# Kernel tuning notes

Measured on AMD Instinct MI355X. Metric: run time of the kernel, lower is better.

Reference implementation:

```python
import math
import jax, jax.numpy as jnp
import numpy as np

B, T, C = 2, 2048, 1024
H, HKV, HD = 16, 4, 64  # n_head, n_kv_head, head_dim
G = H // HKV            # GQA groups
WS = 1024               # sliding window size
GATE_CH = 32


def setup_inputs() -> dict:
    key = jax.random.key(0)
    ks = jax.random.split(key, 8)
    x = jax.random.normal(ks[0], (B, T, C), dtype=jnp.float32)
    ve = jax.random.normal(ks[1], (B, T, HKV * HD), dtype=jnp.float32)
    # realistic RoPE tables: half head_dim frequencies
    d = HD // 2
    inv_freq = 1.0 / (10000.0 ** (jnp.arange(d, dtype=jnp.float32) / d))
    angles = jnp.arange(T, dtype=jnp.float32)[:, None] * inv_freq[None, :]  # (T, d)
    cos = jnp.cos(angles)[None, :, None, :]  # (1, T, 1, d)
    sin = jnp.sin(angles)[None, :, None, :]
    s = 0.02
    Wq = s * jax.random.normal(ks[2], (C, H * HD), dtype=jnp.float32)
    Wk = s * jax.random.normal(ks[3], (C, HKV * HD), dtype=jnp.float32)
    Wv = s * jax.random.normal(ks[4], (C, HKV * HD), dtype=jnp.float32)
    Wproj = s * jax.random.normal(ks[5], (C, C), dtype=jnp.float32)
    Wg = s * jax.random.normal(ks[6], (GATE_CH, HKV), dtype=jnp.float32)
    return {"x": x, "ve": ve, "cos": cos, "sin": sin,
            "Wq": Wq, "Wk": Wk, "Wv": Wv, "Wproj": Wproj, "Wg": Wg, "ws": WS}


def _rope(u, cos, sin):
    d = u.shape[-1] // 2
    u1, u2 = u[..., :d], u[..., d:]
    return jnp.concatenate([u1 * cos + u2 * sin, -u1 * sin + u2 * cos], axis=-1)


def _rmsnorm(u):
    eps = jnp.finfo(u.dtype).eps
    return u * jax.lax.rsqrt(jnp.mean(u * u, axis=-1, keepdims=True) + eps)


def reference(x, ve, cos, sin, Wq, Wk, Wv, Wproj, Wg, ws):
    b, t, c = x.shape
    q = (x @ Wq).reshape(b, t, H, HD)
    k = (x @ Wk).reshape(b, t, HKV, HD)
    v = (x @ Wv).reshape(b, t, HKV, HD)
    # value-embedding gate: 2*sigmoid over first 32 channels of x
    gate = 2.0 * jax.nn.sigmoid(x[..., :GATE_CH] @ Wg)  # (b, t, HKV)
    v = v + gate[..., None] * ve.reshape(b, t, HKV, HD)
    q = _rmsnorm(_rope(q, cos, sin))
    k = _rmsnorm(_rope(k, cos, sin))
    # GQA: view q as (b, t, HKV, G, HD), contract against shared k/v per kv-head
    qg = q.reshape(b, t, HKV, G, HD)
    scale = 1.0 / math.sqrt(HD)
    scores = jnp.einsum('bqhgd,bkhd->bhgqk', qg, k) * scale  # (b, HKV, G, t, t)
    pos = jnp.arange(t)
    # key j attends iff i - ws + 1 <= j <= i (sliding causal window)
    mask = (pos[None, :] >= pos[:, None] - ws + 1) & (pos[None, :] <= pos[:, None])
    scores = jnp.where(mask[None, None, None], scores, -jnp.inf)
    attn = jax.nn.softmax(scores, axis=-1)
    y = jnp.einsum('bhgqk,bkhd->bqhgd', attn, v).reshape(b, t, H * HD)
    return y @ Wproj
```

## Files before the change

kernel.cpp:

```cpp
#include <hip/hip_runtime.h>
#include <hip/hip_bf16.h>

#define Bq 2
#define Tq 2048
#define Cq 1024
#define Hq 16
#define HKVq 4
#define HDq 64
#define Gq 4
#define WSq 1024
#define GATE_CHq 32

typedef __attribute__((ext_vector_type(8))) short short8;
typedef __attribute__((ext_vector_type(4))) float f32x4;
typedef __attribute__((ext_vector_type(2))) unsigned int u32x2;
typedef unsigned int u32;
typedef unsigned short u16;

#if __has_builtin(__builtin_amdgcn_exp2f)
#define EXP2(x) __builtin_amdgcn_exp2f(x)
#else
#define EXP2(x) exp2f(x)
#endif

__device__ __forceinline__ u16 f2bf(float f) {
  u32 u = __float_as_uint(f);
  u32 r = (u + 0x7FFFu + ((u >> 16) & 1u)) >> 16;
  return (u16)r;
}
__device__ __forceinline__ float bf2f(u16 u) {
  return __uint_as_float(((u32)u) << 16);
}

__device__ __forceinline__ void gl_lds16(const u16* g, u16* l) {
  __builtin_amdgcn_global_load_lds(
      (const u32 __attribute__((address_space(1)))*)g,
      (u32 __attribute__((address_space(3)))*)l, 16, 0, 0);
}

template <bool BF16OUT>
__global__ __launch_bounds__(256) void gemm_bt(
    const u16* __restrict__ A, const u16* __restrict__ Bt,
    void* __restrict__ Cv, int M, int N, int K) {
  __shared__ __attribute__((aligned(16))) u16 As[64 * 32];
  __shared__ __attribute__((aligned(16))) u16 Bs[128 * 32];

  const int bm0 = blockIdx.y * 64, bn0 = blockIdx.x * 128;
  const int tid = threadIdx.x;
  const int w = tid >> 6, lane = tid & 63;
  const int wm = (w >> 1) * 32, wn = (w & 1) * 64;
  const int quad = lane >> 4, l16 = lane & 15;

  f32x4 acc[2][4];
#pragma unroll
  for (int mt = 0; mt < 2; mt++)
#pragma unroll
    for (int nt = 0; nt < 4; nt++) acc[mt][nt] = (f32x4){0.f, 0.f, 0.f, 0.f};

  const int mA = tid >> 2, gpA = tid & 3;
  const int goffA = mA * K + (gpA ^ ((mA >> 1) & 3)) * 8;
  int goffB[2];
#pragma unroll
  for (int i = 0; i < 2; i++) {
    int s = i * 256 + tid;
    int m = s >> 2, gp = s & 3;
    goffB[i] = m * K + (gp ^ ((m >> 1) & 3)) * 8;
  }
  const u16* Ab = A + (long)bm0 * K;
  const u16* Bb = Bt + (long)bn0 * K;

  const u16* pA[2];
  const u16* pB[4];
#pragma unroll
  for (int t = 0; t < 2; t++) {
    int ml = wm + t * 16 + l16;
    pA[t] = &As[(ml * 4 + (quad ^ ((ml >> 1) & 3))) * 8];
  }
#pragma unroll
  for (int t = 0; t < 4; t++) {
    int nl = wn + t * 16 + l16;
    pB[t] = &Bs[(nl * 4 + (quad ^ ((nl >> 1) & 3))) * 8];
  }

  for (int k0 = 0; k0 < K; k0 += 32) {
    __syncthreads();
    gl_lds16(Ab + goffA + k0, &As[(w * 64) * 8]);
#pragma unroll
    for (int i = 0; i < 2; i++)
      gl_lds16(Bb + goffB[i] + k0, &Bs[(i * 256 + w * 64) * 8]);
    __syncthreads();

    short8 af[2], bf[4];
#pragma unroll
    for (int t = 0; t < 2; t++) af[t] = *(const short8*)pA[t];
#pragma unroll
    for (int t = 0; t < 4; t++) bf[t] = *(const short8*)pB[t];
#pragma unroll
    for (int mt = 0; mt < 2; mt++)
#pragma unroll
      for (int nt = 0; nt < 4; nt++)
        acc[mt][nt] = __builtin_amdgcn_mfma_f32_16x16x32_bf16(
            af[mt], bf[nt], acc[mt][nt], 0, 0, 0);
  }

#pragma unroll
  for (int mt = 0; mt < 2; mt++)
#pragma unroll
    for (int nt = 0; nt < 4; nt++) {
      int row0 = bm0 + wm + mt * 16 + quad * 4;
      int col = bn0 + wn + nt * 16 + l16;
#pragma unroll
      for (int r = 0; r < 4; r++) {
        if (BF16OUT)
          ((u16*)Cv)[(long)(row0 + r) * N + col] = f2bf(acc[mt][nt][r]);
        else
          ((float*)Cv)[(long)(row0 + r) * N + col] = acc[mt][nt][r];
      }
    }
}

__global__ __launch_bounds__(256) void cast_bf16(const float* __restrict__ S,
                                                 u16* __restrict__ D) {
  int i = (blockIdx.x * 256 + threadIdx.x) * 8;
  float4 a = *(const float4*)(S + i);
  float4 b = *(const float4*)(S + i + 4);
  union { short8 v; u16 u[8]; } o;
  o.u[0] = f2bf(a.x); o.u[1] = f2bf(a.y); o.u[2] = f2bf(a.z); o.u[3] = f2bf(a.w);
  o.u[4] = f2bf(b.x); o.u[5] = f2bf(b.y); o.u[6] = f2bf(b.z); o.u[7] = f2bf(b.w);
  *(short8*)(D + i) = o.v;
}

__device__ __forceinline__ void wtrans_body(const float* __restrict__ S,
                                            u16* __restrict__ D, int N, int n0,
                                            int k0, float (*tile)[65]) {
  int tid = threadIdx.x;
#pragma unroll
  for (int i = 0; i < 16; i++) {
    int idx = i * 256 + tid;
    int kl = idx >> 6, nl = idx & 63;
    tile[kl][nl] = S[(long)(k0 + kl) * N + n0 + nl];
  }
  __syncthreads();
#pragma unroll
  for (int i = 0; i < 16; i++) {
    int idx = i * 256 + tid;
    int nl = idx >> 6, kl = idx & 63;
    D[(long)(n0 + nl) * 1024 + k0 + kl] = f2bf(tile[kl][nl]);
  }
}

__global__ __launch_bounds__(256) void wtrans_all(
    const float* __restrict__ Wq, const float* __restrict__ Wk,
    const float* __restrict__ Wv, const float* __restrict__ Wproj,
    u16* __restrict__ Dqkv, u16* __restrict__ Dproj) {
  __shared__ float tile[64][65];
  int bx = blockIdx.x;
  const float* S;
  u16* Dst;
  int N, nb;
  if (bx < 16)      { S = Wq;    N = 1024; nb = bx;      Dst = Dqkv; }
  else if (bx < 20) { S = Wk;    N = 256;  nb = bx - 16; Dst = Dqkv + 1024 * 1024; }
  else if (bx < 24) { S = Wv;    N = 256;  nb = bx - 20; Dst = Dqkv + 1280 * 1024; }
  else              { S = Wproj; N = 1024; nb = bx - 24; Dst = Dproj; }
  wtrans_body(S, Dst, N, nb * 64, blockIdx.y * 64, tile);
}

__device__ __forceinline__ float rope_rms(float u, int lane, float c, float s) {
  float up = __shfl_xor(u, 32);
  float r = (lane < 32) ? (u * c + up * s) : (u * c - up * s);
  float sum = r * r;
#pragma unroll
  for (int off = 32; off >= 1; off >>= 1) sum += __shfl_xor(sum, off);
  return r * rsqrtf(sum * (1.f / 64.f) + 1.1920928955078125e-07f);
}

__global__ __launch_bounds__(256) void postproc(
    const float* __restrict__ x, const float* __restrict__ ve,
    const float* __restrict__ cosp, const float* __restrict__ sinp,
    const float* __restrict__ Wg, const u16* __restrict__ QKV,
    u16* __restrict__ Qb, u16* __restrict__ Kb, u16* __restrict__ Vb) {
  int bt = blockIdx.x;
  int b = bt >> 11;
  int t = bt & (Tq - 1);
  int tid = threadIdx.x;
  int w = tid >> 6;
  int lane = tid & 63;
  const u16* row = QKV + (long)bt * 1536;

  float c = cosp[t * 32 + (lane & 31)];
  float s = sinp[t * 32 + (lane & 31)];

  float pg = 0.f;
  if (lane < 32) pg = x[(long)bt * Cq + lane] * Wg[lane * HKVq + w];
#pragma unroll
  for (int off = 16; off >= 1; off >>= 1) pg += __shfl_xor(pg, off);
  float z = __shfl(pg, 0);
  float gate = 2.f / (1.f + expf(-z));

  long vi = (long)bt * (HKVq * HDq) + w * HDq + lane;
  float v = bf2f(row[1280 + w * HDq + lane]) + gate * ve[vi];
  Vb[((long)((b * 4 + w) * Tq + t)) * 64 + lane] = f2bf(v);

  float kv = rope_rms(bf2f(row[1024 + w * HDq + lane]), lane, c, s);
  Kb[((long)((b * 4 + w) * Tq + t)) * 64 + lane] = f2bf(kv);

#pragma unroll
  for (int hi = 0; hi < 4; hi++) {
    int h = hi * 4 + w;
    float q = rope_rms(bf2f(row[h * HDq + lane]), lane, c, s);
    Qb[((long)(((b * 4 + hi) * 4 + w) * Tq + t)) * 64 + lane] = f2bf(q);
  }
}

__global__ __launch_bounds__(256) void vtrans(const u16* __restrict__ Vb,
                                              u16* __restrict__ Vtb) {
  __shared__ u16 tile[64][74];
  int bh = blockIdx.y;
  int t0 = blockIdx.x * 64;
  int tid = threadIdx.x;
  const u16* src = Vb + ((long)bh * Tq + t0) * 64;
  u16* dst = Vtb + (long)bh * 64 * Tq + t0;
#pragma unroll
  for (int i = 0; i < 16; i++) {
    int idx = i * 256 + tid;
    int r = idx >> 6, cl = idx & 63;
    tile[r][cl] = src[(long)r * 64 + cl];
  }
  __syncthreads();
#pragma unroll
  for (int i = 0; i < 16; i++) {
    int idx = i * 256 + tid;
    int d = idx >> 6, t = idx & 63;
    dst[(long)d * Tq + t] = tile[t][d];
  }
}

#define CEXP 0.18033688011112042f
#define CEXP8 1.4426950408889634f

template <bool MASK>
__device__ __forceinline__ void attn_tile32(
    int k0, int q0, int quad, int l16, const u16* __restrict__ Ks,
    const u16* __restrict__ Vts, u32* __restrict__ myPs,
    const short8 (&QB)[2][2], f32x4 (&O)[2][4], float (&lsum)[2]) {
  f32x4 S4[4][2];
#pragma unroll
  for (int kt4 = 0; kt4 < 4; kt4++) {
    int key = kt4 * 16 + l16;
    short8 kb0 = *(const short8*)(&Ks[key * 64 + ((quad ^ (key & 7)) * 8)]);
    short8 kb1 = *(const short8*)(&Ks[key * 64 + (((quad + 4) ^ (key & 7)) * 8)]);
#pragma unroll
    for (int qj = 0; qj < 2; qj++) {
      f32x4 acc = (f32x4){0.f, 0.f, 0.f, 0.f};
      acc = __builtin_amdgcn_mfma_f32_16x16x32_bf16(kb0, QB[qj][0], acc, 0, 0, 0);
      acc = __builtin_amdgcn_mfma_f32_16x16x32_bf16(kb1, QB[qj][1], acc, 0, 0, 0);
      S4[kt4][qj] = acc;
    }
  }

#pragma unroll
  for (int kt4 = 0; kt4 < 4; kt4++)
#pragma unroll
    for (int qj = 0; qj < 2; qj++) {
      float Pv[4];
#pragma unroll
      for (int r = 0; r < 4; r++) {
        float sv = S4[kt4][qj][r];
        if (MASK) {
          int kpos = k0 + kt4 * 16 + quad * 4 + r;
          int qpos = q0 + qj * 16 + l16;
          bool valid = (kpos <= qpos) && (kpos >= qpos - (WSq - 1));
          sv = valid ? sv : -1e30f;
        }
        float p = EXP2(__builtin_fmaf(sv, CEXP, -CEXP8));
        Pv[r] = p;
        lsum[qj] += p;
      }
      u32x2 pk;
#pragma unroll
      for (int rp = 0; rp < 2; rp++) {
        u32 lo = __float_as_uint(Pv[2 * rp]) + 0x8000u;
        u32 hi = __float_as_uint(Pv[2 * rp + 1]) + 0x8000u;
        pk[rp] = __builtin_amdgcn_perm(hi, lo, 0x07060302u);
      }
      *(u32x2*)(&myPs[(qj * 16 + l16) * 36 + kt4 * 8 + quad * 2]) = pk;
    }

  short8 vb[4][2];
#pragma unroll
  for (int nt = 0; nt < 4; nt++) {
    int d = nt * 16 + l16;
    vb[nt][0] = *(const short8*)(&Vts[d * 64 + ((quad ^ (d & 7)) * 8)]);
    vb[nt][1] = *(const short8*)(&Vts[d * 64 + (((quad + 4) ^ (d & 7)) * 8)]);
  }

#pragma unroll
  for (int qj = 0; qj < 2; qj++) {
    const u32* prow = &myPs[(qj * 16 + l16) * 36];
    short8 pa0 = *(const short8*)(prow + quad * 4);
    short8 pa1 = *(const short8*)(prow + 16 + quad * 4);
#pragma unroll
    for (int nt = 0; nt < 4; nt++) {
      O[qj][nt] =
          __builtin_amdgcn_mfma_f32_16x16x32_bf16(pa0, vb[nt][0], O[qj][nt], 0, 0, 0);
      O[qj][nt] =
          __builtin_amdgcn_mfma_f32_16x16x32_bf16(pa1, vb[nt][1], O[qj][nt], 0, 0, 0);
    }
  }
}

__global__ __launch_bounds__(256, 2) void attn_mfma(
    const u16* __restrict__ Qb, const u16* __restrict__ Kb,
    const u16* __restrict__ Vtb, u16* __restrict__ Yb) {
  __shared__ __attribute__((aligned(16))) u16 Ks[64 * 64];
  __shared__ __attribute__((aligned(16))) u16 Vts[64 * 64];
  __shared__ __attribute__((aligned(16))) u32 Ps[4][32 * 36];

  int bid = blockIdx.x;
  int bh = bid & 7;
  int qt32 = bid >> 3;
  int hkv = bh & 3;
  int b = bh >> 2;
  int q0 = qt32 * 32;
  int tid = threadIdx.x;
  int g = tid >> 6;
  int lane = tid & 63;
  int quad = lane >> 4;
  int l16 = lane & 15;

  short8 QB[2][2];
#pragma unroll
  for (int qj = 0; qj < 2; qj++) {
    const u16* qb = Qb +
        ((long)(((b * 4 + hkv) * 4 + g) * Tq + q0 + qj * 16 + l16)) * 64 +
        quad * 8;
    QB[qj][0] = *(const short8*)(qb);
    QB[qj][1] = *(const short8*)(qb + 32);
  }

  f32x4 O[2][4];
#pragma unroll
  for (int qj = 0; qj < 2; qj++)
#pragma unroll
    for (int nt = 0; nt < 4; nt++) O[qj][nt] = (f32x4){0.f, 0.f, 0.f, 0.f};
  float lsum[2] = {0.f, 0.f};

  int lo = q0 - (WSq - 1);
  int st = (lo < 0 ? 0 : lo) >> 6;
  int et = (q0 + 31) >> 6;

  const u16* Kbase = Kb + ((long)((b * 4 + hkv) * Tq)) * 64;
  const u16* Vbase = Vtb + ((long)((b * 4 + hkv) * 64)) * Tq;
  u32* myPs = &Ps[g][0];

  int rowoffK[2], rowoffV[2];
#pragma unroll
  for (int i = 0; i < 2; i++) {
    int s = i * 256 + tid;
    int row = s >> 3, gl = s & 7;
    rowoffK[i] = row * 64 + (gl ^ (row & 7)) * 8;
    rowoffV[i] = row * Tq + (gl ^ (row & 7)) * 8;
  }

  for (int kt = st; kt <= et; kt++) {
    int k0 = kt * 64;
    __syncthreads();
#pragma unroll
    for (int i = 0; i < 2; i++) {
      gl_lds16(Kbase + (long)k0 * 64 + rowoffK[i], &Ks[(i * 256 + g * 64) * 8]);
      gl_lds16(Vbase + k0 + rowoffV[i], &Vts[(i * 256 + g * 64) * 8]);
    }
    __syncthreads();

    bool needC = (k0 > q0 - 63);
    bool needW = (k0 < q0 - 992);
    if (needC || needW)
      attn_tile32<true>(k0, q0, quad, l16, Ks, Vts, myPs, QB, O, lsum);
    else
      attn_tile32<false>(k0, q0, quad, l16, Ks, Vts, myPs, QB, O, lsum);
  }

#pragma unroll
  for (int qj = 0; qj < 2; qj++) {
    lsum[qj] += __shfl_xor(lsum[qj], 16);
    lsum[qj] += __shfl_xor(lsum[qj], 32);
  }

  int h = hkv * 4 + g;
#pragma unroll
  for (int qj = 0; qj < 2; qj++) {
    float invl[4];
#pragma unroll
    for (int r = 0; r < 4; r++) invl[r] = 1.f / __shfl(lsum[qj], quad * 4 + r);
#pragma unroll
    for (int nt = 0; nt < 4; nt++)
#pragma unroll
      for (int r = 0; r < 4; r++)
        Yb[((long)(b * Tq + q0 + qj * 16 + quad * 4 + r)) * 1024 + h * 64 +
           nt * 16 + l16] = f2bf(O[qj][nt][r] * invl[r]);
  }
}

extern "C" void kernel_launch(void* const* d_in, const int* in_sizes, int n_in,
                              void* d_out, int out_size, void* d_ws,
                              size_t ws_size, hipStream_t stream) {
  const float* x     = (const float*)d_in[0];
  const float* ve    = (const float*)d_in[1];
  const float* cosp  = (const float*)d_in[2];
  const float* sinp  = (const float*)d_in[3];
  const float* Wq    = (const float*)d_in[4];
  const float* Wk    = (const float*)d_in[5];
  const float* Wv    = (const float*)d_in[6];
  const float* Wproj = (const float*)d_in[7];
  const float* Wg    = (const float*)d_in[8];

  char* base = (char*)d_ws;
  u16* xb     = (u16*)(base);
  u16* Qb     = xb;
  u16* WqkvT  = (u16*)(base + 8388608);
  u16* Kb     = WqkvT;
  u16* WprojT = (u16*)(base + 11534336);
  u16* QKVb   = (u16*)(base + 13631488);
  u16* Vb     = (u16*)(base + 26214400);
  u16* Vtb    = (u16*)(base + 28311552);
  u16* Yb     = (u16*)(base + 30408704);
  float* out = (float*)d_out;

  cast_bf16<<<2048, 256, 0, stream>>>(x, xb);
  wtrans_all<<<dim3(40, 16), 256, 0, stream>>>(Wq, Wk, Wv, Wproj, WqkvT,
                                               WprojT);
  gemm_bt<true><<<dim3(12, 64), 256, 0, stream>>>(xb, WqkvT, QKVb, 4096, 1536,
                                                  1024);
  postproc<<<Bq * Tq, 256, 0, stream>>>(x, ve, cosp, sinp, Wg, QKVb, Qb, Kb,
                                        Vb);
  vtrans<<<dim3(32, 8), 256, 0, stream>>>(Vb, Vtb);
  attn_mfma<<<512, 256, 0, stream>>>(Qb, Kb, Vtb, Yb);
  gemm_bt<false><<<dim3(8, 64), 256, 0, stream>>>(Yb, WprojT, out, 4096, 1024,
                                                  1024);
}
```

Before: 186.2 us.

## Fuse prep kernels, merge V transpose into postproc, deepen GEMM and attention K tiles

Merges the x cast and weight transpose into one launch, and folds the V transpose into the postprocessing kernel through an LDS tile. The intermediate V buffer and two launches go away. The GEMM K step grows from 32 to 64 and the attention key tile from 64 to 128, halving the barrier and load rounds per unit of work. In exchange LDS use per block rises in attention, which may cut occupancy. Postproc now runs far fewer, serial per-block loops.

```diff
diff --git a/kernel.cpp b/kernel.cpp
--- a/kernel.cpp
+++ b/kernel.cpp
@@ -42,8 +42,8 @@
 __global__ __launch_bounds__(256) void gemm_bt(
     const u16* __restrict__ A, const u16* __restrict__ Bt,
     void* __restrict__ Cv, int M, int N, int K) {
-  __shared__ __attribute__((aligned(16))) u16 As[64 * 32];
-  __shared__ __attribute__((aligned(16))) u16 Bs[128 * 32];
+  __shared__ __attribute__((aligned(16))) u16 As[64 * 64];
+  __shared__ __attribute__((aligned(16))) u16 Bs[128 * 64];
 
   const int bm0 = blockIdx.y * 64, bn0 = blockIdx.x * 128;
   const int tid = threadIdx.x;
@@ -57,50 +57,52 @@
 #pragma unroll
     for (int nt = 0; nt < 4; nt++) acc[mt][nt] = (f32x4){0.f, 0.f, 0.f, 0.f};
 
-  const int mA = tid >> 2, gpA = tid & 3;
-  const int goffA = mA * K + (gpA ^ ((mA >> 1) & 3)) * 8;
-  int goffB[2];
+  int goffA[2], goffB[4];
 #pragma unroll
   for (int i = 0; i < 2; i++) {
     int s = i * 256 + tid;
-    int m = s >> 2, gp = s & 3;
-    goffB[i] = m * K + (gp ^ ((m >> 1) & 3)) * 8;
+    int m = s >> 3, gp = s & 7;
+    goffA[i] = m * K + (gp ^ (m & 7)) * 8;
+  }
+#pragma unroll
+  for (int i = 0; i < 4; i++) {
+    int s = i * 256 + tid;
+    int m = s >> 3, gp = s & 7;
+    goffB[i] = m * K + (gp ^ (m & 7)) * 8;
   }
   const u16* Ab = A + (long)bm0 * K;
   const u16* Bb = Bt + (long)bn0 * K;
 
-  const u16* pA[2];
-  const u16* pB[4];
-#pragma unroll
-  for (int t = 0; t < 2; t++) {
-    int ml = wm + t * 16 + l16;
-    pA[t] = &As[(ml * 4 + (quad ^ ((ml >> 1) & 3))) * 8];
-  }
-#pragma unroll
-  for (int t = 0; t < 4; t++) {
-    int nl = wn + t * 16 + l16;
-    pB[t] = &Bs[(nl * 4 + (quad ^ ((nl >> 1) & 3))) * 8];
-  }
-
-  for (int k0 = 0; k0 < K; k0 += 32) {
+  for (int k0 = 0; k0 < K; k0 += 64) {
     __syncthreads();
-    gl_lds16(Ab + goffA + k0, &As[(w * 64) * 8]);
 #pragma unroll
     for (int i = 0; i < 2; i++)
+      gl_lds16(Ab + goffA[i] + k0, &As[(i * 256 + w * 64) * 8]);
+#pragma unroll
+    for (int i = 0; i < 4; i++)
       gl_lds16(Bb + goffB[i] + k0, &Bs[(i * 256 + w * 64) * 8]);
     __syncthreads();
 
-    short8 af[2], bf[4];
-#pragma unroll
-    for (int t = 0; t < 2; t++) af[t] = *(const short8*)pA[t];
-#pragma unroll
-    for (int t = 0; t < 4; t++) bf[t] = *(const short8*)pB[t];
-#pragma unroll
-    for (int mt = 0; mt < 2; mt++)
-#pragma unroll
-      for (int nt = 0; nt < 4; nt++)
-        acc[mt][nt] = __builtin_amdgcn_mfma_f32_16x16x32_bf16(
-            af[mt], bf[nt], acc[mt][nt], 0, 0, 0);
+#pragma unroll
+    for (int ks = 0; ks < 2; ks++) {
+      short8 af[2], bf[4];
+#pragma unroll
+      for (int mt = 0; mt < 2; mt++) {
+        int ml = wm + mt * 16 + l16;
+        af[mt] = *(const short8*)&As[ml * 64 + (((ks * 4 + quad) ^ (ml & 7)) * 8)];
+      }
+#pragma unroll
+      for (int nt = 0; nt < 4; nt++) {
+        int nl = wn + nt * 16 + l16;
+        bf[nt] = *(const short8*)&Bs[nl * 64 + (((ks * 4 + quad) ^ (nl & 7)) * 8)];
+      }
+#pragma unroll
+      for (int mt = 0; mt < 2; mt++)
+#pragma unroll
+        for (int nt = 0; nt < 4; nt++)
+          acc[mt][nt] = __builtin_amdgcn_mfma_f32_16x16x32_bf16(
+              af[mt], bf[nt], acc[mt][nt], 0, 0, 0);
+    }
   }
 
 #pragma unroll
@@ -119,50 +121,48 @@
     }
 }
 
-__global__ __launch_bounds__(256) void cast_bf16(const float* __restrict__ S,
-                                                 u16* __restrict__ D) {
-  int i = (blockIdx.x * 256 + threadIdx.x) * 8;
-  float4 a = *(const float4*)(S + i);
-  float4 b = *(const float4*)(S + i + 4);
-  union { short8 v; u16 u[8]; } o;
-  o.u[0] = f2bf(a.x); o.u[1] = f2bf(a.y); o.u[2] = f2bf(a.z); o.u[3] = f2bf(a.w);
-  o.u[4] = f2bf(b.x); o.u[5] = f2bf(b.y); o.u[6] = f2bf(b.z); o.u[7] = f2bf(b.w);
-  *(short8*)(D + i) = o.v;
-}
-
-__device__ __forceinline__ void wtrans_body(const float* __restrict__ S,
-                                            u16* __restrict__ D, int N, int n0,
-                                            int k0, float (*tile)[65]) {
-  int tid = threadIdx.x;
-#pragma unroll
-  for (int i = 0; i < 16; i++) {
-    int idx = i * 256 + tid;
-    int kl = idx >> 6, nl = idx & 63;
-    tile[kl][nl] = S[(long)(k0 + kl) * N + n0 + nl];
-  }
-  __syncthreads();
-#pragma unroll
-  for (int i = 0; i < 16; i++) {
-    int idx = i * 256 + tid;
-    int nl = idx >> 6, kl = idx & 63;
-    D[(long)(n0 + nl) * 1024 + k0 + kl] = f2bf(tile[kl][nl]);
-  }
-}
-
-__global__ __launch_bounds__(256) void wtrans_all(
+__global__ __launch_bounds__(256) void prep(
+    const float* __restrict__ x, u16* __restrict__ xb,
     const float* __restrict__ Wq, const float* __restrict__ Wk,
     const float* __restrict__ Wv, const float* __restrict__ Wproj,
     u16* __restrict__ Dqkv, u16* __restrict__ Dproj) {
   __shared__ float tile[64][65];
   int bx = blockIdx.x;
+  int tid = threadIdx.x;
+  if (bx < 2048) {
+    int i = (bx * 256 + tid) * 8;
+    float4 a = *(const float4*)(x + i);
+    float4 b = *(const float4*)(x + i + 4);
+    union { short8 v; u16 u[8]; } o;
+    o.u[0] = f2bf(a.x); o.u[1] = f2bf(a.y); o.u[2] = f2bf(a.z); o.u[3] = f2bf(a.w);
+    o.u[4] = f2bf(b.x); o.u[5] = f2bf(b.y); o.u[6] = f2bf(b.z); o.u[7] = f2bf(b.w);
+    *(short8*)(xb + i) = o.v;
+    return;
+  }
+  int wb = bx - 2048;
+  int obx = wb >> 4;
+  int k0 = (wb & 15) * 64;
   const float* S;
   u16* Dst;
   int N, nb;
-  if (bx < 16)      { S = Wq;    N = 1024; nb = bx;      Dst = Dqkv; }
-  else if (bx < 20) { S = Wk;    N = 256;  nb = bx - 16; Dst = Dqkv + 1024 * 1024; }
-  else if (bx < 24) { S = Wv;    N = 256;  nb = bx - 20; Dst = Dqkv + 1280 * 1024; }
-  else              { S = Wproj; N = 1024; nb = bx - 24; Dst = Dproj; }
-  wtrans_body(S, Dst, N, nb * 64, blockIdx.y * 64, tile);
+  if (obx < 16)      { S = Wq;    N = 1024; nb = obx;      Dst = Dqkv; }
+  else if (obx < 20) { S = Wk;    N = 256;  nb = obx - 16; Dst = Dqkv + 1024 * 1024; }
+  else if (obx < 24) { S = Wv;    N = 256;  nb = obx - 20; Dst = Dqkv + 1280 * 1024; }
+  else               { S = Wproj; N = 1024; nb = obx - 24; Dst = Dproj; }
+  int n0 = nb * 64;
+#pragma unroll
+  for (int i = 0; i < 16; i++) {
+    int idx = i * 256 + tid;
+    int kl = idx >> 6, nl = idx & 63;
+    tile[kl][nl] = S[(long)(k0 + kl) * N + n0 + nl];
+  }
+  __syncthreads();
+#pragma unroll
+  for (int i = 0; i < 16; i++) {
+    int idx = i * 256 + tid;
+    int nl = idx >> 6, kl = idx & 63;
+    Dst[(long)(n0 + nl) * 1024 + k0 + kl] = f2bf(tile[kl][nl]);
+  }
 }
 
 __device__ __forceinline__ float rope_rms(float u, int lane, float c, float s) {
@@ -174,64 +174,51 @@
   return r * rsqrtf(sum * (1.f / 64.f) + 1.1920928955078125e-07f);
 }
 
-__global__ __launch_bounds__(256) void postproc(
+__global__ __launch_bounds__(256) void postproc2(
     const float* __restrict__ x, const float* __restrict__ ve,
     const float* __restrict__ cosp, const float* __restrict__ sinp,
     const float* __restrict__ Wg, const u16* __restrict__ QKV,
-    u16* __restrict__ Qb, u16* __restrict__ Kb, u16* __restrict__ Vb) {
-  int bt = blockIdx.x;
-  int b = bt >> 11;
-  int t = bt & (Tq - 1);
-  int tid = threadIdx.x;
-  int w = tid >> 6;
-  int lane = tid & 63;
-  const u16* row = QKV + (long)bt * 1536;
-
-  float c = cosp[t * 32 + (lane & 31)];
-  float s = sinp[t * 32 + (lane & 31)];
-
-  float pg = 0.f;
-  if (lane < 32) pg = x[(long)bt * Cq + lane] * Wg[lane * HKVq + w];
-#pragma unroll
-  for (int off = 16; off >= 1; off >>= 1) pg += __shfl_xor(pg, off);
-  float z = __shfl(pg, 0);
-  float gate = 2.f / (1.f + expf(-z));
-
-  long vi = (long)bt * (HKVq * HDq) + w * HDq + lane;
-  float v = bf2f(row[1280 + w * HDq + lane]) + gate * ve[vi];
-  Vb[((long)((b * 4 + w) * Tq + t)) * 64 + lane] = f2bf(v);
-
-  float kv = rope_rms(bf2f(row[1024 + w * HDq + lane]), lane, c, s);
-  Kb[((long)((b * 4 + w) * Tq + t)) * 64 + lane] = f2bf(kv);
-
-#pragma unroll
-  for (int hi = 0; hi < 4; hi++) {
-    int h = hi * 4 + w;
-    float q = rope_rms(bf2f(row[h * HDq + lane]), lane, c, s);
-    Qb[((long)(((b * 4 + hi) * 4 + w) * Tq + t)) * 64 + lane] = f2bf(q);
-  }
-}
-
-__global__ __launch_bounds__(256) void vtrans(const u16* __restrict__ Vb,
-                                              u16* __restrict__ Vtb) {
-  __shared__ u16 tile[64][74];
+    u16* __restrict__ Qb, u16* __restrict__ Kb, u16* __restrict__ Vtb) {
+  __shared__ u16 vt[64][70];
   int bh = blockIdx.y;
+  int b = bh >> 2, hkv = bh & 3;
   int t0 = blockIdx.x * 64;
   int tid = threadIdx.x;
-  const u16* src = Vb + ((long)bh * Tq + t0) * 64;
-  u16* dst = Vtb + (long)bh * 64 * Tq + t0;
+  int w = tid >> 6, lane = tid & 63;
+
+  for (int tt = 0; tt < 16; tt++) {
+    int tl = tt * 4 + w;
+    int t = t0 + tl;
+    long bt = (long)b * Tq + t;
+    const u16* row = QKV + bt * 1536;
+    float c = cosp[t * 32 + (lane & 31)];
+    float s = sinp[t * 32 + (lane & 31)];
+
+    float pg = 0.f;
+    if (lane < 32) pg = x[bt * Cq + lane] * Wg[lane * HKVq + hkv];
+#pragma unroll
+    for (int off = 16; off >= 1; off >>= 1) pg += __shfl_xor(pg, off);
+    float gate = 2.f / (1.f + expf(-__shfl(pg, 0)));
+
+    float v = bf2f(row[1280 + hkv * 64 + lane]) +
+              gate * ve[bt * 256 + hkv * 64 + lane];
+    vt[tl][lane] = f2bf(v);
+
+    float kv = rope_rms(bf2f(row[1024 + hkv * 64 + lane]), lane, c, s);
+    Kb[((long)bh * Tq + t) * 64 + lane] = f2bf(kv);
+
+#pragma unroll
+    for (int g = 0; g < 4; g++) {
+      float q = rope_rms(bf2f(row[(hkv * 4 + g) * 64 + lane]), lane, c, s);
+      Qb[((long)(bh * 4 + g) * Tq + t) * 64 + lane] = f2bf(q);
+    }
+  }
+  __syncthreads();
 #pragma unroll
   for (int i = 0; i < 16; i++) {
     int idx = i * 256 + tid;
-    int r = idx >> 6, cl = idx & 63;
-    tile[r][cl] = src[(long)r * 64 + cl];
-  }
-  __syncthreads();
-#pragma unroll
-  for (int i = 0; i < 16; i++) {
-    int idx = i * 256 + tid;
-    int d = idx >> 6, t = idx & 63;
-    dst[(long)d * Tq + t] = tile[t][d];
+    int d = idx >> 6, tl = idx & 63;
+    Vtb[(long)bh * 64 * Tq + (long)d * Tq + t0 + tl] = vt[tl][d];
   }
 }
 
@@ -239,16 +226,17 @@
 #define CEXP8 1.4426950408889634f
 
 template <bool MASK>
-__device__ __forceinline__ void attn_tile32(
-    int k0, int q0, int quad, int l16, const u16* __restrict__ Ks,
-    const u16* __restrict__ Vts, u32* __restrict__ myPs,
-    const short8 (&QB)[2][2], f32x4 (&O)[2][4], float (&lsum)[2]) {
+__device__ __forceinline__ void attn_half(
+    int k0h, int key_base, int vg_base, int q0, int quad, int l16,
+    const u16* __restrict__ Ks, const u16* __restrict__ Vts,
+    u32* __restrict__ myPs, const short8 (&QB)[2][2], f32x4 (&O)[2][4],
+    float (&lsum)[2]) {
   f32x4 S4[4][2];
 #pragma unroll
   for (int kt4 = 0; kt4 < 4; kt4++) {
-    int key = kt4 * 16 + l16;
+    int key = key_base + kt4 * 16 + l16;
     short8 kb0 = *(const short8*)(&Ks[key * 64 + ((quad ^ (key & 7)) * 8)]);
-    short8 kb1 = *(const short8*)(&Ks[key * 64 + (((quad + 4) ^ (key & 7)) * 8)]);
+    short8 kb1 = *(const short8*)(&Ks[key * 64 + (((4 + quad) ^ (key & 7)) * 8)]);
 #pragma unroll
     for (int qj = 0; qj < 2; qj++) {
       f32x4 acc = (f32x4){0.f, 0.f, 0.f, 0.f};
@@ -267,7 +255,7 @@
       for (int r = 0; r < 4; r++) {
         float sv = S4[kt4][qj][r];
         if (MASK) {
-          int kpos = k0 + kt4 * 16 + quad * 4 + r;
+          int kpos = k0h + kt4 * 16 + quad * 4 + r;
           int qpos = q0 + qj * 16 + l16;
           bool valid = (kpos <= qpos) && (kpos >= qpos - (WSq - 1));
           sv = valid ? sv : -1e30f;
@@ -290,8 +278,9 @@
 #pragma unroll
   for (int nt = 0; nt < 4; nt++) {
     int d = nt * 16 + l16;
-    vb[nt][0] = *(const short8*)(&Vts[d * 64 + ((quad ^ (d & 7)) * 8)]);
-    vb[nt][1] = *(const short8*)(&Vts[d * 64 + (((quad + 4) ^ (d & 7)) * 8)]);
+    vb[nt][0] = *(const short8*)(&Vts[d * 128 + (((vg_base + quad) ^ (d & 7)) * 8)]);
+    vb[nt][1] =
+        *(const short8*)(&Vts[d * 128 + (((vg_base + 4 + quad) ^ (d & 7)) * 8)]);
   }
 
 #pragma unroll
@@ -312,9 +301,9 @@
 __global__ __launch_bounds__(256, 2) void attn_mfma(
     const u16* __restrict__ Qb, const u16* __restrict__ Kb,
     const u16* __restrict__ Vtb, u16* __restrict__ Yb) {
-  __shared__ __attribute__((aligned(16))) u16 Ks[64 * 64];
-  __shared__ __attribute__((aligned(16))) u16 Vts[64 * 64];
-  __shared__ __attribute__((aligned(16))) u32 Ps[4][32 * 36];
+  __shared__ __attribute__((aligned(16))) u16 Ks[128 * 64];
+  __shared__ __attribute__((aligned(16))) u16 Vts[64 * 128];
+  __shared__ __attribute__((aligned(16))) u32 Ps[4][2][32 * 36];
 
   int bid = blockIdx.x;
   int bh = bid & 7;
@@ -331,9 +320,8 @@
   short8 QB[2][2];
 #pragma unroll
   for (int qj = 0; qj < 2; qj++) {
-    const u16* qb = Qb +
-        ((long)(((b * 4 + hkv) * 4 + g) * Tq + q0 + qj * 16 + l16)) * 64 +
-        quad * 8;
+    const u16* qb =
+        Qb + ((long)((bh * 4 + g) * Tq + q0 + qj * 16 + l16)) * 64 + quad * 8;
     QB[qj][0] = *(const short8*)(qb);
     QB[qj][1] = *(const short8*)(qb + 32);
   }
@@ -346,38 +334,44 @@
   float lsum[2] = {0.f, 0.f};
 
   int lo = q0 - (WSq - 1);
-  int st = (lo < 0 ? 0 : lo) >> 6;
-  int et = (q0 + 31) >> 6;
-
-  const u16* Kbase = Kb + ((long)((b * 4 + hkv) * Tq)) * 64;
-  const u16* Vbase = Vtb + ((long)((b * 4 + hkv) * 64)) * Tq;
-  u32* myPs = &Ps[g][0];
-
-  int rowoffK[2], rowoffV[2];
-#pragma unroll
-  for (int i = 0; i < 2; i++) {
+  int st = (lo < 0 ? 0 : lo) >> 7;
+  int et = (q0 + 31) >> 7;
+
+  const u16* Kbase = Kb + ((long)bh * Tq) * 64;
+  const u16* Vbase = Vtb + ((long)bh * 64) * Tq;
+
+  int rowoffK[4], rowoffV[4];
+#pragma unroll
+  for (int i = 0; i < 4; i++) {
     int s = i * 256 + tid;
-    int row = s >> 3, gl = s & 7;
-    rowoffK[i] = row * 64 + (gl ^ (row & 7)) * 8;
-    rowoffV[i] = row * Tq + (gl ^ (row & 7)) * 8;
+    int kr = s >> 3, kgp = s & 7;
+    rowoffK[i] = kr * 64 + (kgp ^ (kr & 7)) * 8;
+    int d = s >> 4, vgp = s & 15;
+    rowoffV[i] = d * Tq + (vgp ^ (d & 7)) * 8;
   }
 
   for (int kt = st; kt <= et; kt++) {
-    int k0 = kt * 64;
+    int k0 = kt << 7;
     __syncthreads();
 #pragma unroll
-    for (int i = 0; i < 2; i++) {
+    for (int i = 0; i < 4; i++) {
       gl_lds16(Kbase + (long)k0 * 64 + rowoffK[i], &Ks[(i * 256 + g * 64) * 8]);
       gl_lds16(Vbase + k0 + rowoffV[i], &Vts[(i * 256 + g * 64) * 8]);
     }
     __syncthreads();
 
-    bool needC = (k0 > q0 - 63);
+    bool needC = (k0 + 127 > q0);
     bool needW = (k0 < q0 - 992);
-    if (needC || needW)
-      attn_tile32<true>(k0, q0, quad, l16, Ks, Vts, myPs, QB, O, lsum);
-    else
-      attn_tile32<false>(k0, q0, quad, l16, Ks, Vts, myPs, QB, O, lsum);
+    if (needC || needW) {
+      attn_half<true>(k0, 0, 0, q0, quad, l16, Ks, Vts, &Ps[g][0][0], QB, O, lsum);
+      attn_half<true>(k0 + 64, 64, 8, q0, quad, l16, Ks, Vts, &Ps[g][1][0], QB,
+                      O, lsum);
+    } else {
+      attn_half<false>(k0, 0, 0, q0, quad, l16, Ks, Vts, &Ps[g][0][0], QB, O,
+                       lsum);
+      attn_half<false>(k0 + 64, 64, 8, q0, quad, l16, Ks, Vts, &Ps[g][1][0], QB,
+                       O, lsum);
+    }
   }
 
 #pragma unroll
@@ -421,19 +415,15 @@
   u16* Kb     = WqkvT;
   u16* WprojT = (u16*)(base + 11534336);
   u16* QKVb   = (u16*)(base + 13631488);
-  u16* Vb     = (u16*)(base + 26214400);
-  u16* Vtb    = (u16*)(base + 28311552);
-  u16* Yb     = (u16*)(base + 30408704);
+  u16* Vtb    = (u16*)(base + 26214400);
+  u16* Yb     = (u16*)(base + 28311552);
   float* out = (float*)d_out;
 
-  cast_bf16<<<2048, 256, 0, stream>>>(x, xb);
-  wtrans_all<<<dim3(40, 16), 256, 0, stream>>>(Wq, Wk, Wv, Wproj, WqkvT,
-                                               WprojT);
+  prep<<<2688, 256, 0, stream>>>(x, xb, Wq, Wk, Wv, Wproj, WqkvT, WprojT);
   gemm_bt<true><<<dim3(12, 64), 256, 0, stream>>>(xb, WqkvT, QKVb, 4096, 1536,
                                                   1024);
-  postproc<<<Bq * Tq, 256, 0, stream>>>(x, ve, cosp, sinp, Wg, QKVb, Qb, Kb,
-                                        Vb);
-  vtrans<<<dim3(32, 8), 256, 0, stream>>>(Vb, Vtb);
+  postproc2<<<dim3(32, 8), 256, 0, stream>>>(x, ve, cosp, sinp, Wg, QKVb, Qb,
+                                             Kb, Vtb);
   attn_mfma<<<512, 256, 0, stream>>>(Qb, Kb, Vtb, Yb);
   gemm_bt<false><<<dim3(8, 64), 256, 0, stream>>>(Yb, WprojT, out, 4096, 1024,
                                                   1024);
```

Measured after the change: 183.2 us. Within noise of the previous version (-1.6%).
